# Kernel tuning notes

Hardware: AMD Instinct MI355X
Metric: run time of the kernel (lower is better)

Reference implementation:

```python
import jax, jax.numpy as jnp
import numpy as np

N_NODES = 100000
N_EDGES = 1600000
VOCAB = 1000
EMB_DIM = 64
OUT_DIM = 32


def setup_inputs() -> dict:
    key = jax.random.key(0)
    k1, k2, k3, k4, k5 = jax.random.split(key, 5)
    node_seq = jax.random.randint(k1, (N_NODES,), 0, VOCAB, dtype=jnp.int64)
    edge_index = jax.random.randint(k2, (2, N_EDGES), 0, N_NODES, dtype=jnp.int64)
    edge_weight = jax.random.uniform(k3, (N_EDGES,), dtype=jnp.float32)
    emb = jax.random.normal(k4, (VOCAB, EMB_DIM), dtype=jnp.float32)
    W = jax.random.normal(k5, (EMB_DIM, OUT_DIM), dtype=jnp.float32) * (1.0 / np.sqrt(EMB_DIM))
    b = jnp.zeros((OUT_DIM,), dtype=jnp.float32)
    return {"node_seq": node_seq, "edge_index": edge_index, "edge_weight": edge_weight,
            "emb": emb, "W": W, "b": b}


def reference(node_seq, edge_index, edge_weight, emb, W, b):
    N = node_seq.shape[0]
    # Embedding lookup: [N, EMB_DIM]
    x = emb[node_seq]
    # Linear transform first (GCNConv applies lin before propagate): [N, OUT_DIM]
    xw = x @ W
    # Add self loops with weight 1 (PyG GCNConv default add_self_loops=True, fill_value=1)
    loop = jnp.arange(N, dtype=edge_index.dtype)
    row = jnp.concatenate([edge_index[0], loop])
    col = jnp.concatenate([edge_index[1], loop])
    w = jnp.concatenate([edge_weight, jnp.ones((N,), dtype=edge_weight.dtype)])
    # Symmetric gcn_norm: deg over targets, norm = d^{-1/2}[row] * w * d^{-1/2}[col]
    deg = jax.ops.segment_sum(w, col, num_segments=N)
    dis = jnp.where(deg > 0, jax.lax.rsqrt(jnp.where(deg > 0, deg, 1.0)), 0.0)
    norm = dis[row] * w * dis[col]
    # Gather messages from source nodes, scale, scatter-add into targets
    msgs = norm[:, None] * xw[row]            # [E+N, OUT_DIM]
    out = jax.ops.segment_sum(msgs, col, num_segments=N) + b  # [N, OUT_DIM]
    # Mean pool over nodes
    return out.mean(axis=0)
```

## Files before the change

kernel.cpp:

```cpp
#include <hip/hip_runtime.h>

#define N_NODES 100000
#define N_EDGES 1600000
#define VOCAB   1000
#define EMB_DIM 64
#define OUT_DIM 32

#define BKT_BITS 9
#define BKT_SIZE 512
#define NBKT ((N_NODES + BKT_SIZE - 1) / BKT_SIZE)
#define CAP  12288
#define NSB  512
#define CHUNK (N_EDGES / NSB)

#define NBC 256
#define TBC 512

__device__ __forceinline__ void fatomic_add(float* p, float v) {
    unsafeAtomicAdd(p, v);
}

__global__ void k_init(int* __restrict__ cursors) {
    int i = blockIdx.x * blockDim.x + threadIdx.x;
    if (i < 2 * NBKT) cursors[i] = (i < NBKT ? i : i - NBKT) * CAP;
}

__global__ void __launch_bounds__(256) k_scatter2(
        const int* __restrict__ row, const int* __restrict__ col,
        const float* __restrict__ w, int* __restrict__ cursors,
        uint2* __restrict__ colrec, uint2* __restrict__ rowrec) {
    __shared__ int cC[NBKT], cR[NBKT], bC[NBKT], bR[NBKT];
    for (int i = threadIdx.x; i < NBKT; i += 256) { cC[i] = 0; cR[i] = 0; }
    __syncthreads();
    const int e0 = blockIdx.x * CHUNK;
    for (int i = threadIdx.x; i < CHUNK; i += 256) {
        atomicAdd(&cC[col[e0 + i] >> BKT_BITS], 1);
        atomicAdd(&cR[row[e0 + i] >> BKT_BITS], 1);
    }
    __syncthreads();
    for (int i = threadIdx.x; i < NBKT; i += 256) {
        bC[i] = atomicAdd(&cursors[i], cC[i]);
        bR[i] = atomicAdd(&cursors[NBKT + i], cR[i]);
        cC[i] = 0; cR[i] = 0;
    }
    __syncthreads();
    for (int i = threadIdx.x; i < CHUNK; i += 256) {
        int c = col[e0 + i];
        int r = row[e0 + i];
        unsigned ww = __float_as_uint(w[e0 + i]);
        int pb = c >> BKT_BITS;
        colrec[bC[pb] + atomicAdd(&cC[pb], 1)] =
            make_uint2((unsigned)(c & (BKT_SIZE - 1)), ww);
        int rb = r >> BKT_BITS;
        rowrec[bR[rb] + atomicAdd(&cR[rb], 1)] =
            make_uint2((unsigned)c | ((unsigned)(r & (BKT_SIZE - 1)) << 17), ww);
    }
}

__global__ void __launch_bounds__(256) k_bucket_dis(
        const uint2* __restrict__ colrec, const int* __restrict__ cursors,
        float* __restrict__ dis) {
    __shared__ float acc[BKT_SIZE];
    const int b = blockIdx.x;
    for (int i = threadIdx.x; i < BKT_SIZE; i += 256) acc[i] = 0.0f;
    __syncthreads();
    const int base = b * CAP;
    const int cnt = cursors[b] - base;
    for (int i = threadIdx.x; i < cnt; i += 256) {
        uint2 r = colrec[base + i];
        fatomic_add(&acc[r.x], __uint_as_float(r.y));
    }
    __syncthreads();
    const int n0 = b << BKT_BITS;
    for (int i = threadIdx.x; i < BKT_SIZE && n0 + i < N_NODES; i += 256)
        dis[n0 + i] = __frsqrt_rn(1.0f + acc[i]);
}

__global__ void __launch_bounds__(512) k_bucket_coeff(
        const uint2* __restrict__ rowrec, const int* __restrict__ cursors,
        const float* __restrict__ dis, const int* __restrict__ node_seq,
        float* __restrict__ gcoeff) {
    __shared__ float sacc[BKT_SIZE];
    __shared__ float lc[VOCAB];
    const int b = blockIdx.x;
    for (int i = threadIdx.x; i < BKT_SIZE; i += 512) sacc[i] = 0.0f;
    for (int i = threadIdx.x; i < VOCAB; i += 512) lc[i] = 0.0f;
    __syncthreads();
    const int base = b * CAP;
    const int cnt = cursors[NBKT + b] - base;
    for (int i = threadIdx.x; i < cnt; i += 512) {
        uint2 rec = rowrec[base + i];
        int c  = rec.x & 0x1FFFF;
        int lr = rec.x >> 17;
        fatomic_add(&sacc[lr], __uint_as_float(rec.y) * dis[c]);
    }
    __syncthreads();
    const int n0 = b << BKT_BITS;
    for (int i = threadIdx.x; i < BKT_SIZE; i += 512) {
        int n = n0 + i;
        if (n < N_NODES) {
            float d = dis[n];
            fatomic_add(&lc[node_seq[n]], d * (sacc[i] + d));
        }
    }
    __syncthreads();
    for (int i = threadIdx.x; i < VOCAB; i += 512)
        gcoeff[b * VOCAB + i] = lc[i];
}

__global__ void k_init_deg(float* __restrict__ deg) {
    int i = blockIdx.x * blockDim.x + threadIdx.x;
    if (i < N_NODES) deg[i] = 1.0f;
}
__global__ void k_deg(const int* __restrict__ col, const float* __restrict__ w,
                      float* __restrict__ deg) {
    int i = blockIdx.x * blockDim.x + threadIdx.x;
    if (i < N_EDGES) fatomic_add(&deg[col[i]], w[i]);
}
__global__ void k_dis(float* __restrict__ deg) {
    int i = blockIdx.x * blockDim.x + threadIdx.x;
    if (i < N_NODES) deg[i] = __frsqrt_rn(deg[i]);
}
__global__ void __launch_bounds__(TBC) k_coeff_stream(
        const int* __restrict__ row, const int* __restrict__ col,
        const float* __restrict__ w, const float* __restrict__ dis,
        const int* __restrict__ node_seq, float* __restrict__ gcoeff) {
    __shared__ float lc[VOCAB];
    for (int i = threadIdx.x; i < VOCAB; i += TBC) lc[i] = 0.0f;
    __syncthreads();
    const int total = N_EDGES + N_NODES;
    const int stride = NBC * TBC;
    for (int i = blockIdx.x * TBC + threadIdx.x; i < total; i += stride) {
        if (i < N_EDGES) {
            int r = row[i];
            fatomic_add(&lc[node_seq[r]], dis[r] * w[i] * dis[col[i]]);
        } else {
            int n = i - N_EDGES;
            float d = dis[n];
            fatomic_add(&lc[node_seq[n]], d * d);
        }
    }
    __syncthreads();
    for (int i = threadIdx.x; i < VOCAB; i += TBC)
        gcoeff[blockIdx.x * VOCAB + i] = lc[i];
}

__global__ void __launch_bounds__(256) k_reduce(
        const float* __restrict__ gcoeff, float* __restrict__ coeff, int npart) {
    int g = blockIdx.x * 256 + threadIdx.x;
    int v = g >> 6;
    int l = g & 63;
    if (v >= VOCAB) return;
    float s = 0.0f;
    for (int p = l; p < npart; p += 64) s += gcoeff[p * VOCAB + v];
    for (int off = 32; off > 0; off >>= 1) s += __shfl_down(s, off, 64);
    if (l == 0) coeff[v] = s;
}

__global__ void __launch_bounds__(1024) k_final(
        const float* __restrict__ coeff, const float* __restrict__ emb,
        const float* __restrict__ W, const float* __restrict__ bias,
        float* __restrict__ out) {
    __shared__ float lc[VOCAB];
    __shared__ float tk[16 * 64];
    int t = threadIdx.x;
    for (int v = t; v < VOCAB; v += 1024) lc[v] = coeff[v];
    __syncthreads();

    int k = t & 63;
    int g = t >> 6;
    float p = 0.0f;
    for (int v = g; v < VOCAB; v += 16) p += lc[v] * emb[v * EMB_DIM + k];
    tk[g * 64 + k] = p;
    __syncthreads();

    if (t < 64) {
        float s = 0.0f;
        for (int gg = 0; gg < 16; ++gg) s += tk[gg * 64 + t];
        tk[t] = s;
    }
    __syncthreads();

    if (t < OUT_DIM) {
        float s = 0.0f;
        for (int kk = 0; kk < EMB_DIM; ++kk) s += tk[kk] * W[kk * OUT_DIM + t];
        out[t] = s * (1.0f / (float)N_NODES) + bias[t];
    }
}

extern "C" void kernel_launch(void* const* d_in, const int* in_sizes, int n_in,
                              void* d_out, int out_size, void* d_ws, size_t ws_size,
                              hipStream_t stream) {
    const int*   node_seq = (const int*)  d_in[0];
    const int*   eidx     = (const int*)  d_in[1];
    const float* ew       = (const float*)d_in[2];
    const float* emb      = (const float*)d_in[3];
    const float* W        = (const float*)d_in[4];
    const float* b        = (const float*)d_in[5];
    float*       out      = (float*)d_out;

    const int* row = eidx;
    const int* col = eidx + N_EDGES;

    char* wsb = (char*)d_ws;
    const size_t REC_BYTES = (size_t)NBKT * CAP * sizeof(uint2);
    const size_t need = 2 * REC_BYTES + 4096 + (size_t)N_NODES * 4
                      + (size_t)NBKT * VOCAB * 4 + VOCAB * 4 + 4096;

    if (ws_size >= need) {
        uint2* colrec  = (uint2*)wsb;
        uint2* rowrec  = (uint2*)(wsb + REC_BYTES);
        int*   cursors = (int*)(wsb + 2 * REC_BYTES);
        float* dis     = (float*)(wsb + 2 * REC_BYTES + 4096);
        float* gcoeff  = dis + N_NODES;
        float* coeff   = gcoeff + (size_t)NBKT * VOCAB;

        k_init<<<2, 256, 0, stream>>>(cursors);
        k_scatter2<<<NSB, 256, 0, stream>>>(row, col, ew, cursors, colrec, rowrec);
        k_bucket_dis<<<NBKT, 256, 0, stream>>>(colrec, cursors, dis);
        k_bucket_coeff<<<NBKT, 512, 0, stream>>>(rowrec, cursors, dis, node_seq, gcoeff);
        k_reduce<<<(VOCAB * 64 + 255) / 256, 256, 0, stream>>>(gcoeff, coeff, NBKT);
        k_final<<<1, 1024, 0, stream>>>(coeff, emb, W, b, out);
    } else {
        float* dis    = (float*)wsb;
        float* gcoeff = dis + N_NODES;
        float* coeff  = gcoeff + (size_t)NBC * VOCAB;

        k_init_deg<<<(N_NODES + 255) / 256, 256, 0, stream>>>(dis);
        k_deg<<<(N_EDGES + 255) / 256, 256, 0, stream>>>(col, ew, dis);
        k_dis<<<(N_NODES + 255) / 256, 256, 0, stream>>>(dis);
        k_coeff_stream<<<NBC, TBC, 0, stream>>>(row, col, ew, dis, node_seq, gcoeff);
        k_reduce<<<(VOCAB * 64 + 255) / 256, 256, 0, stream>>>(gcoeff, coeff, NBC);
        k_final<<<1, 1024, 0, stream>>>(coeff, emb, W, b, out);
    }
}
```

Before: 163.7 us.

## Bucket edges only by target and stage scatter in shared memory

Drops the second row-bucketed record stream. Every edge is now bucketed once by target column, with the source row packed into the record. The scatter kernel does a block-local prefix sum and stages records in LDS so global writes go out contiguously per bucket. The coefficient kernel gathers dis and node_seq for the source row from a packed disseq array and accumulates straight into per-vocab LDS bins. This halves record writes and reads, but the coefficient pass now does random global gathers of disseq per edge instead of a bucket-local reduction, and it adds more shared memory per scatter block.

```diff
diff --git a/kernel.cpp b/kernel.cpp
--- a/kernel.cpp
+++ b/kernel.cpp
@@ -22,44 +22,58 @@
 
 __global__ void k_init(int* __restrict__ cursors) {
     int i = blockIdx.x * blockDim.x + threadIdx.x;
-    if (i < 2 * NBKT) cursors[i] = (i < NBKT ? i : i - NBKT) * CAP;
-}
-
-__global__ void __launch_bounds__(256) k_scatter2(
+    if (i < NBKT) cursors[i] = i * CAP;
+}
+
+__global__ void __launch_bounds__(256) k_scatter(
         const int* __restrict__ row, const int* __restrict__ col,
         const float* __restrict__ w, int* __restrict__ cursors,
-        uint2* __restrict__ colrec, uint2* __restrict__ rowrec) {
-    __shared__ int cC[NBKT], cR[NBKT], bC[NBKT], bR[NBKT];
-    for (int i = threadIdx.x; i < NBKT; i += 256) { cC[i] = 0; cR[i] = 0; }
-    __syncthreads();
+        uint2* __restrict__ recs) {
+    __shared__ uint2 stage[CHUNK];
+    __shared__ unsigned char seg[CHUNK];
+    __shared__ int cnt[NBKT], lofs[NBKT], gbase[NBKT];
+    __shared__ int sc[256];
+    const int tid = threadIdx.x;
     const int e0 = blockIdx.x * CHUNK;
-    for (int i = threadIdx.x; i < CHUNK; i += 256) {
-        atomicAdd(&cC[col[e0 + i] >> BKT_BITS], 1);
-        atomicAdd(&cR[row[e0 + i] >> BKT_BITS], 1);
-    }
-    __syncthreads();
-    for (int i = threadIdx.x; i < NBKT; i += 256) {
-        bC[i] = atomicAdd(&cursors[i], cC[i]);
-        bR[i] = atomicAdd(&cursors[NBKT + i], cR[i]);
-        cC[i] = 0; cR[i] = 0;
-    }
-    __syncthreads();
-    for (int i = threadIdx.x; i < CHUNK; i += 256) {
+
+    for (int i = tid; i < NBKT; i += 256) cnt[i] = 0;
+    __syncthreads();
+    for (int i = tid; i < CHUNK; i += 256)
+        atomicAdd(&cnt[col[e0 + i] >> BKT_BITS], 1);
+    __syncthreads();
+    sc[tid] = (tid < NBKT) ? cnt[tid] : 0;
+    __syncthreads();
+    for (int d = 1; d < 256; d <<= 1) {
+        int v = (tid >= d) ? sc[tid - d] : 0;
+        __syncthreads();
+        sc[tid] += v;
+        __syncthreads();
+    }
+    if (tid < NBKT) {
+        lofs[tid]  = sc[tid] - cnt[tid];
+        gbase[tid] = atomicAdd(&cursors[tid], cnt[tid]);
+        cnt[tid]   = 0;
+    }
+    __syncthreads();
+    for (int i = tid; i < CHUNK; i += 256) {
         int c = col[e0 + i];
         int r = row[e0 + i];
-        unsigned ww = __float_as_uint(w[e0 + i]);
-        int pb = c >> BKT_BITS;
-        colrec[bC[pb] + atomicAdd(&cC[pb], 1)] =
-            make_uint2((unsigned)(c & (BKT_SIZE - 1)), ww);
-        int rb = r >> BKT_BITS;
-        rowrec[bR[rb] + atomicAdd(&cR[rb], 1)] =
-            make_uint2((unsigned)c | ((unsigned)(r & (BKT_SIZE - 1)) << 17), ww);
-    }
-}
-
-__global__ void __launch_bounds__(256) k_bucket_dis(
-        const uint2* __restrict__ colrec, const int* __restrict__ cursors,
-        float* __restrict__ dis) {
+        int b = c >> BKT_BITS;
+        int p = lofs[b] + atomicAdd(&cnt[b], 1);
+        stage[p] = make_uint2(((unsigned)r << BKT_BITS) | (unsigned)(c & (BKT_SIZE - 1)),
+                              __float_as_uint(w[e0 + i]));
+        seg[p] = (unsigned char)b;
+    }
+    __syncthreads();
+    for (int i = tid; i < CHUNK; i += 256) {
+        int b = seg[i];
+        recs[gbase[b] + (i - lofs[b])] = stage[i];
+    }
+}
+
+__global__ void __launch_bounds__(256) k_dis(
+        const uint2* __restrict__ recs, const int* __restrict__ cursors,
+        const int* __restrict__ node_seq, uint2* __restrict__ disseq) {
     __shared__ float acc[BKT_SIZE];
     const int b = blockIdx.x;
     for (int i = threadIdx.x; i < BKT_SIZE; i += 256) acc[i] = 0.0f;
@@ -67,40 +81,45 @@
     const int base = b * CAP;
     const int cnt = cursors[b] - base;
     for (int i = threadIdx.x; i < cnt; i += 256) {
-        uint2 r = colrec[base + i];
-        fatomic_add(&acc[r.x], __uint_as_float(r.y));
+        uint2 r = recs[base + i];
+        fatomic_add(&acc[r.x & (BKT_SIZE - 1)], __uint_as_float(r.y));
     }
     __syncthreads();
     const int n0 = b << BKT_BITS;
     for (int i = threadIdx.x; i < BKT_SIZE && n0 + i < N_NODES; i += 256)
-        dis[n0 + i] = __frsqrt_rn(1.0f + acc[i]);
-}
-
-__global__ void __launch_bounds__(512) k_bucket_coeff(
-        const uint2* __restrict__ rowrec, const int* __restrict__ cursors,
-        const float* __restrict__ dis, const int* __restrict__ node_seq,
-        float* __restrict__ gcoeff) {
-    __shared__ float sacc[BKT_SIZE];
+        disseq[n0 + i] = make_uint2(__float_as_uint(__frsqrt_rn(1.0f + acc[i])),
+                                    (unsigned)node_seq[n0 + i]);
+}
+
+__global__ void __launch_bounds__(512) k_coeff(
+        const uint2* __restrict__ recs, const int* __restrict__ cursors,
+        const uint2* __restrict__ disseq, float* __restrict__ gcoeff) {
+    __shared__ float dloc[BKT_SIZE];
     __shared__ float lc[VOCAB];
     const int b = blockIdx.x;
-    for (int i = threadIdx.x; i < BKT_SIZE; i += 512) sacc[i] = 0.0f;
+    const int n0 = b << BKT_BITS;
     for (int i = threadIdx.x; i < VOCAB; i += 512) lc[i] = 0.0f;
+    if (threadIdx.x < BKT_SIZE) {
+        int n = n0 + threadIdx.x;
+        dloc[threadIdx.x] = (n < N_NODES) ? __uint_as_float(disseq[n].x) : 0.0f;
+    }
     __syncthreads();
     const int base = b * CAP;
-    const int cnt = cursors[NBKT + b] - base;
+    const int cnt = cursors[b] - base;
     for (int i = threadIdx.x; i < cnt; i += 512) {
-        uint2 rec = rowrec[base + i];
-        int c  = rec.x & 0x1FFFF;
-        int lr = rec.x >> 17;
-        fatomic_add(&sacc[lr], __uint_as_float(rec.y) * dis[c]);
-    }
-    __syncthreads();
-    const int n0 = b << BKT_BITS;
-    for (int i = threadIdx.x; i < BKT_SIZE; i += 512) {
-        int n = n0 + i;
+        uint2 rec = recs[base + i];
+        int lcol = rec.x & (BKT_SIZE - 1);
+        int r    = rec.x >> BKT_BITS;
+        uint2 ds = disseq[r];
+        float norm = __uint_as_float(ds.x) * __uint_as_float(rec.y) * dloc[lcol];
+        fatomic_add(&lc[ds.y], norm);
+    }
+    if (threadIdx.x < BKT_SIZE) {
+        int n = n0 + threadIdx.x;
         if (n < N_NODES) {
-            float d = dis[n];
-            fatomic_add(&lc[node_seq[n]], d * (sacc[i] + d));
+            uint2 ds = disseq[n];
+            float d = __uint_as_float(ds.x);
+            fatomic_add(&lc[ds.y], d * d);
         }
     }
     __syncthreads();
@@ -117,7 +136,7 @@
     int i = blockIdx.x * blockDim.x + threadIdx.x;
     if (i < N_EDGES) fatomic_add(&deg[col[i]], w[i]);
 }
-__global__ void k_dis(float* __restrict__ deg) {
+__global__ void k_dis_fb(float* __restrict__ deg) {
     int i = blockIdx.x * blockDim.x + threadIdx.x;
     if (i < N_NODES) deg[i] = __frsqrt_rn(deg[i]);
 }
@@ -204,21 +223,20 @@
 
     char* wsb = (char*)d_ws;
     const size_t REC_BYTES = (size_t)NBKT * CAP * sizeof(uint2);
-    const size_t need = 2 * REC_BYTES + 4096 + (size_t)N_NODES * 4
+    const size_t need = REC_BYTES + 4096 + (size_t)N_NODES * 8
                       + (size_t)NBKT * VOCAB * 4 + VOCAB * 4 + 4096;
 
     if (ws_size >= need) {
-        uint2* colrec  = (uint2*)wsb;
-        uint2* rowrec  = (uint2*)(wsb + REC_BYTES);
-        int*   cursors = (int*)(wsb + 2 * REC_BYTES);
-        float* dis     = (float*)(wsb + 2 * REC_BYTES + 4096);
-        float* gcoeff  = dis + N_NODES;
+        uint2* recs    = (uint2*)wsb;
+        int*   cursors = (int*)(wsb + REC_BYTES);
+        uint2* disseq  = (uint2*)(wsb + REC_BYTES + 4096);
+        float* gcoeff  = (float*)(disseq + N_NODES);
         float* coeff   = gcoeff + (size_t)NBKT * VOCAB;
 
-        k_init<<<2, 256, 0, stream>>>(cursors);
-        k_scatter2<<<NSB, 256, 0, stream>>>(row, col, ew, cursors, colrec, rowrec);
-        k_bucket_dis<<<NBKT, 256, 0, stream>>>(colrec, cursors, dis);
-        k_bucket_coeff<<<NBKT, 512, 0, stream>>>(rowrec, cursors, dis, node_seq, gcoeff);
+        k_init<<<1, 256, 0, stream>>>(cursors);
+        k_scatter<<<NSB, 256, 0, stream>>>(row, col, ew, cursors, recs);
+        k_dis<<<NBKT, 256, 0, stream>>>(recs, cursors, node_seq, disseq);
+        k_coeff<<<NBKT, 512, 0, stream>>>(recs, cursors, disseq, gcoeff);
         k_reduce<<<(VOCAB * 64 + 255) / 256, 256, 0, stream>>>(gcoeff, coeff, NBKT);
         k_final<<<1, 1024, 0, stream>>>(coeff, emb, W, b, out);
     } else {
@@ -228,7 +246,7 @@
 
         k_init_deg<<<(N_NODES + 255) / 256, 256, 0, stream>>>(dis);
         k_deg<<<(N_EDGES + 255) / 256, 256, 0, stream>>>(col, ew, dis);
-        k_dis<<<(N_NODES + 255) / 256, 256, 0, stream>>>(dis);
+        k_dis_fb<<<(N_NODES + 255) / 256, 256, 0, stream>>>(dis);
         k_coeff_stream<<<NBC, TBC, 0, stream>>>(row, col, ew, dis, node_seq, gcoeff);
         k_reduce<<<(VOCAB * 64 + 255) / 256, 256, 0, stream>>>(gcoeff, coeff, NBC);
         k_final<<<1, 1024, 0, stream>>>(coeff, emb, W, b, out);
```

Measured after the change: 145.6 us. 1.12x faster.
